# Optimization experiments

Hardware: AMD Instinct MI355X
Metric: run time of the kernel (lower is better)

The kernel has to match this reference:

```python
import jax, jax.numpy as jnp
import numpy as np

N_NODES = 50000
N_EDGES = 1600000
D = 128  # in_channels == hidden_channels


def _sage_conv(x, src, dst, W_l, W_r, b, n_nodes):
    # PyG SAGEConv (mean aggr): out = lin_l(mean_{j in N(i)} x_j) + lin_r(x_i)
    msg = x[src]                                              # [E, d] gather
    agg = jax.ops.segment_sum(msg, dst, num_segments=n_nodes)  # [N, d]
    deg = jax.ops.segment_sum(jnp.ones((src.shape[0],), x.dtype), dst,
                              num_segments=n_nodes)            # [N]
    mean = agg / jnp.maximum(deg, 1.0)[:, None]
    return mean @ W_l.T + b + x @ W_r.T


def setup_inputs() -> dict:
    key = jax.random.key(0)
    ks = jax.random.split(key, 8)
    x = jax.random.normal(ks[0], (N_NODES, D), dtype=jnp.float32)
    edge_index = jax.random.randint(ks[1], (2, N_EDGES), 0, N_NODES, dtype=jnp.int32)
    s = 1.0 / np.sqrt(D)
    W1_l = jax.random.uniform(ks[2], (D, D), jnp.float32, -s, s)
    W1_r = jax.random.uniform(ks[3], (D, D), jnp.float32, -s, s)
    b1 = jnp.zeros((D,), jnp.float32)
    W2_l = jax.random.uniform(ks[4], (D, D), jnp.float32, -s, s)
    W2_r = jax.random.uniform(ks[5], (D, D), jnp.float32, -s, s)
    b2 = jnp.zeros((D,), jnp.float32)
    return {"x": x, "edge_index": edge_index,
            "W1_l": W1_l, "W1_r": W1_r, "b1": b1,
            "W2_l": W2_l, "W2_r": W2_r, "b2": b2}


def reference(x, edge_index, W1_l, W1_r, b1, W2_l, W2_r, b2):
    src, dst = edge_index[0], edge_index[1]
    n = x.shape[0]
    # layer 1: conv -> relu (dropout is identity in eval mode)
    h = jax.nn.relu(_sage_conv(x, src, dst, W1_l, W1_r, b1, n))
    # layer 2
    h = jax.nn.relu(_sage_conv(h, src, dst, W2_l, W2_r, b2, n))
    return h
```

## Files before the change

### kernel.cpp

```cpp
#include <hip/hip_runtime.h>

#define D 128
#define BW_LOG 6
#define BWID 64
#define CAP 4096
#define CHUNK 4096
#define NB_MAX 1024

typedef unsigned short u16;
typedef unsigned int u32;
typedef __attribute__((ext_vector_type(8))) short bf16x8;
typedef __attribute__((ext_vector_type(8))) unsigned short u16x8;
typedef __attribute__((ext_vector_type(4))) float f32x4;

__device__ __forceinline__ float bf2f(u16 h) { return __uint_as_float(((u32)h) << 16); }
__device__ __forceinline__ u16 f2bf(float f) {
    u32 u = __float_as_uint(f);
    u32 r = (u + 0x7fffu + ((u >> 16) & 1u)) >> 16;
    return (u16)r;
}


__global__ __launch_bounds__(256)
void prep_kernel(const float* __restrict__ x, u16* __restrict__ xb, int n4,
                 const float* __restrict__ W1l, const float* __restrict__ W1r,
                 const float* __restrict__ W2l, const float* __restrict__ W2r,
                 u16* __restrict__ wc1, u16* __restrict__ wc2,
                 const int* __restrict__ dst, int* __restrict__ gh,
                 int E, int nb, int nblk, int xblk) {
    __shared__ int h[NB_MAX];
    int b = blockIdx.x;
    int t = threadIdx.x;
    if (b < xblk) {
        int i = b * 256 + t;
        if (i < n4) {
            float4 v = ((const float4*)x)[i];
            ushort4 o;
            o.x = f2bf(v.x); o.y = f2bf(v.y); o.z = f2bf(v.z); o.w = f2bf(v.w);
            ((ushort4*)xb)[i] = o;
        }
        return;
    }
    if (b < xblk + 256) {
        int wb = b - xblk;
        int n = wb & 127;
        const float* Wl = (wb < 128) ? W1l : W2l;
        const float* Wr = (wb < 128) ? W1r : W2r;
        u16* wcat = (wb < 128) ? wc1 : wc2;
        float v = (t < 128) ? Wl[n * 128 + t] : Wr[n * 128 + t - 128];
        wcat[n * 256 + t] = f2bf(v);
        return;
    }
    int hb = b - xblk - 256;
    for (int i = t; i < nb; i += 256) h[i] = 0;
    __syncthreads();
    int lo = hb * CHUNK, hi = min(lo + CHUNK, E);
    for (int i = lo + t; i < hi; i += 256) atomicAdd(&h[dst[i] >> BW_LOG], 1);
    __syncthreads();
    for (int i = t; i < nb; i += 256) gh[(size_t)i * nblk + hb] = h[i];
}


__global__ __launch_bounds__(64)
void part_scan1_kernel(int* __restrict__ gh, int* __restrict__ btot, int nblk) {
    int k = blockIdx.x;
    int t = threadIdx.x;
    int* row = gh + (size_t)k * nblk;
    int chunk = (nblk + 63) >> 6;
    int lo = t * chunk, hi = min(lo + chunk, nblk);
    int s = 0;
    for (int i = lo; i < hi; ++i) s += row[i];
    int incl = s;
#pragma unroll
    for (int d2 = 1; d2 < 64; d2 <<= 1) { int u = __shfl_up(incl, d2, 64); if (t >= d2) incl += u; }
    int excl = incl - s;
    for (int i = lo; i < hi; ++i) { int c = row[i]; row[i] = excl; excl += c; }
    if (t == 63) btot[k] = incl;
}

__global__ __launch_bounds__(1024)
void part_scan2_kernel(const int* __restrict__ btot, int* __restrict__ bbase,
                       int nb, int* __restrict__ offN) {
    __shared__ int ws[16];
    int t = threadIdx.x, lane = t & 63, wid = t >> 6;
    int v = (t < nb) ? btot[t] : 0;
    int incl = v;
#pragma unroll
    for (int d2 = 1; d2 < 64; d2 <<= 1) { int u = __shfl_up(incl, d2, 64); if (lane >= d2) incl += u; }
    if (lane == 63) ws[wid] = incl;
    __syncthreads();
    if (wid == 0) {
        int w = (lane < 16) ? ws[lane] : 0;
#pragma unroll
        for (int d2 = 1; d2 < 16; d2 <<= 1) { int u = __shfl_up(w, d2, 64); if (lane >= d2) w += u; }
        if (lane < 16) ws[lane] = w;
    }
    __syncthreads();
    int base = wid ? ws[wid - 1] : 0;
    int excl = base + incl - v;
    if (t < nb) bbase[t] = excl;
    if (t == nb - 1) { bbase[nb] = excl + v; *offN = excl + v; }
}

__global__ __launch_bounds__(256)
void part_scatter_kernel(const int* __restrict__ src, const int* __restrict__ dst,
                         const int* __restrict__ gh, const int* __restrict__ bbase,
                         u32* __restrict__ ebuf, int E, int nb, int nblk) {
    __shared__ int cur[NB_MAX];
    int b = blockIdx.x;
    for (int i = threadIdx.x; i < nb; i += 256)
        cur[i] = bbase[i] + gh[(size_t)i * nblk + b];
    __syncthreads();
    int lo = b * CHUNK, hi = min(lo + CHUNK, E);
    for (int i = lo + threadIdx.x; i < hi; i += 256) {
        int d = dst[i];
        int p = atomicAdd(&cur[d >> BW_LOG], 1);
        ebuf[p] = ((u32)(d & (BWID - 1)) << 16) | (u32)src[i];
    }
}

__global__ __launch_bounds__(256)
void bucket_sort_kernel(u32* __restrict__ ebuf, const int* __restrict__ bbase,
                        int* __restrict__ off, int n_nodes) {
    __shared__ u32 in_s[CAP];
    __shared__ u16 out_s[CAP];
    __shared__ int hist[BWID], cur[BWID];
    int b = blockIdx.x;
    int base = bbase[b];
    int n_b = bbase[b + 1] - base;
    int t = threadIdx.x;
    if (t < BWID) hist[t] = 0;
    for (int i = t; i < n_b && i < CAP; i += 256) in_s[i] = ebuf[base + i];
    __syncthreads();
    for (int i = t; i < n_b && i < CAP; i += 256) atomicAdd(&hist[in_s[i] >> 16], 1);
    __syncthreads();
    if (t < BWID) {
        int s = hist[t];
        int incl = s;
#pragma unroll
        for (int d2 = 1; d2 < 64; d2 <<= 1) { int u = __shfl_up(incl, d2, 64); if (t >= d2) incl += u; }
        int excl = incl - s;
        cur[t] = excl;
        int node = (b << BW_LOG) + t;
        if (node < n_nodes) off[node] = base + excl;
    }
    __syncthreads();
    for (int i = t; i < n_b && i < CAP; i += 256) {
        u32 v = in_s[i];
        int p = atomicAdd(&cur[v >> 16], 1);
        if (p < CAP) out_s[p] = (u16)(v & 0xffffu);
    }
    __syncthreads();
    for (int i = t; i < n_b && i < CAP; i += 256) ebuf[base + i] = (u32)out_s[i];
}


__global__ __launch_bounds__(256)
void aggregate_bf16_kernel(const u16* __restrict__ xb, const int* __restrict__ off,
                           const u32* __restrict__ eidx, u16* __restrict__ meanb,
                           int n_nodes) {
    int node = blockIdx.x * 8 + (threadIdx.x >> 5);
    int lane = threadIdx.x & 31;
    if (node >= n_nodes) return;
    int beg = off[node], end = off[node + 1];
    int c = lane * 4;

    float ax = 0.f, ay = 0.f, az = 0.f, aw = 0.f;
    int e = beg;
    for (; e + 8 <= end; e += 8) {
        ushort4 v0 = *(const ushort4*)&xb[(size_t)eidx[e + 0] * D + c];
        ushort4 v1 = *(const ushort4*)&xb[(size_t)eidx[e + 1] * D + c];
        ushort4 v2 = *(const ushort4*)&xb[(size_t)eidx[e + 2] * D + c];
        ushort4 v3 = *(const ushort4*)&xb[(size_t)eidx[e + 3] * D + c];
        ushort4 v4 = *(const ushort4*)&xb[(size_t)eidx[e + 4] * D + c];
        ushort4 v5 = *(const ushort4*)&xb[(size_t)eidx[e + 5] * D + c];
        ushort4 v6 = *(const ushort4*)&xb[(size_t)eidx[e + 6] * D + c];
        ushort4 v7 = *(const ushort4*)&xb[(size_t)eidx[e + 7] * D + c];
        ax += bf2f(v0.x) + bf2f(v1.x) + bf2f(v2.x) + bf2f(v3.x)
            + bf2f(v4.x) + bf2f(v5.x) + bf2f(v6.x) + bf2f(v7.x);
        ay += bf2f(v0.y) + bf2f(v1.y) + bf2f(v2.y) + bf2f(v3.y)
            + bf2f(v4.y) + bf2f(v5.y) + bf2f(v6.y) + bf2f(v7.y);
        az += bf2f(v0.z) + bf2f(v1.z) + bf2f(v2.z) + bf2f(v3.z)
            + bf2f(v4.z) + bf2f(v5.z) + bf2f(v6.z) + bf2f(v7.z);
        aw += bf2f(v0.w) + bf2f(v1.w) + bf2f(v2.w) + bf2f(v3.w)
            + bf2f(v4.w) + bf2f(v5.w) + bf2f(v6.w) + bf2f(v7.w);
    }
    for (; e < end; ++e) {
        ushort4 v = *(const ushort4*)&xb[(size_t)eidx[e] * D + c];
        ax += bf2f(v.x); ay += bf2f(v.y); az += bf2f(v.z); aw += bf2f(v.w);
    }

    int deg = end - beg;
    float inv = 1.f / (float)(deg > 0 ? deg : 1);
    ushort4 o;
    o.x = f2bf(ax * inv); o.y = f2bf(ay * inv); o.z = f2bf(az * inv); o.w = f2bf(aw * inv);
    *(ushort4*)&meanb[(size_t)node * D + c] = o;
}


template<bool OUT_BF16>
__global__ __launch_bounds__(512)
void linear_mfma_kernel(const u16* __restrict__ Amean, const u16* __restrict__ Aself,
                        const u16* __restrict__ Wc, const float* __restrict__ bias,
                        void* __restrict__ outp, int N) {
    __shared__ u16 ws[128][136];

    int t = threadIdx.x;
    int l = t & 63;
    int wv = t >> 6;
    int m0 = blockIdx.x * 128 + wv * 16;
    int lr = l & 15;
    int kg = (l >> 4) * 8;
    int rowA = m0 + lr;
    int rc = rowA < N ? rowA : N - 1;
    const u16* r1 = Amean + (size_t)rc * D;
    const u16* r2 = Aself + (size_t)rc * D;

    bf16x8 a[8];
#pragma unroll
    for (int kt = 0; kt < 4; ++kt) {
        a[kt]     = *(const bf16x8*)(r1 + kt * 32 + kg);
        a[kt + 4] = *(const bf16x8*)(r2 + kt * 32 + kg);
    }

    f32x4 acc[8];
#pragma unroll
    for (int nt = 0; nt < 8; ++nt) acc[nt] = (f32x4){0.f, 0.f, 0.f, 0.f};

    for (int half = 0; half < 2; ++half) {
        if (half) __syncthreads();
        for (int i = t; i < 2048; i += 512) {
            int n = i >> 4, kq = i & 15;
            *(u16x8*)&ws[n][kq * 8] = *(const u16x8*)&Wc[(size_t)n * 256 + half * 128 + kq * 8];
        }
        __syncthreads();

#pragma unroll
        for (int nt = 0; nt < 8; ++nt) {
            bf16x8 b0 = *(const bf16x8*)&ws[nt * 16 + lr][0 * 32 + kg];
            bf16x8 b1 = *(const bf16x8*)&ws[nt * 16 + lr][1 * 32 + kg];
            bf16x8 b2 = *(const bf16x8*)&ws[nt * 16 + lr][2 * 32 + kg];
            bf16x8 b3 = *(const bf16x8*)&ws[nt * 16 + lr][3 * 32 + kg];
            acc[nt] = __builtin_amdgcn_mfma_f32_16x16x32_bf16(a[half * 4 + 0], b0, acc[nt], 0, 0, 0);
            acc[nt] = __builtin_amdgcn_mfma_f32_16x16x32_bf16(a[half * 4 + 1], b1, acc[nt], 0, 0, 0);
            acc[nt] = __builtin_amdgcn_mfma_f32_16x16x32_bf16(a[half * 4 + 2], b2, acc[nt], 0, 0, 0);
            acc[nt] = __builtin_amdgcn_mfma_f32_16x16x32_bf16(a[half * 4 + 3], b3, acc[nt], 0, 0, 0);
        }
    }

#pragma unroll
    for (int nt = 0; nt < 8; ++nt) {
        int col = nt * 16 + lr;
        float bb = bias[col];
#pragma unroll
        for (int j = 0; j < 4; ++j) {
            int r = m0 + (l >> 4) * 4 + j;
            if (r < N) {
                float v = fmaxf(acc[nt][j] + bb, 0.f);
                if (OUT_BF16) ((u16*)outp)[(size_t)r * D + col] = f2bf(v);
                else          ((float*)outp)[(size_t)r * D + col] = v;
            }
        }
    }
}

extern "C" void kernel_launch(void* const* d_in, const int* in_sizes, int n_in,
                              void* d_out, int out_size, void* d_ws, size_t ws_size,
                              hipStream_t stream) {
    const float* x   = (const float*)d_in[0];
    const int*   ei  = (const int*)d_in[1];
    const float* W1l = (const float*)d_in[2];
    const float* W1r = (const float*)d_in[3];
    const float* b1  = (const float*)d_in[4];
    const float* W2l = (const float*)d_in[5];
    const float* W2r = (const float*)d_in[6];
    const float* b2  = (const float*)d_in[7];
    float* out = (float*)d_out;

    const int N = in_sizes[0] / D;
    const int E = in_sizes[1] / 2;
    const int* src = ei;
    const int* dst = ei + E;
    const int NB = (N + BWID - 1) >> BW_LOG;
    const int NBLK = (E + CHUNK - 1) / CHUNK;
    const int N4 = N * D / 4;
    const int XBLK = (N4 + 255) / 256;

    char* wp_ = (char*)d_ws;
    auto alloc = [&](size_t bytes) { char* p = wp_; wp_ += (bytes + 63) & ~(size_t)63; return p; };
    int* off_p   = (int*)alloc((size_t)(N + 1) * 4);
    int* bbase_p = (int*)alloc((size_t)(NB + 1) * 4);
    int* btot_p  = (int*)alloc((size_t)NB * 4);
    int* gh_p    = (int*)alloc((size_t)NB * NBLK * 4);
    u32* ebuf_p  = (u32*)alloc((size_t)E * 4);
    u16* xb      = (u16*)alloc((size_t)N * D * 2);
    u16* meanb   = (u16*)alloc((size_t)N * D * 2);
    u16* h1b     = (u16*)alloc((size_t)N * D * 2);
    u16* wc1     = (u16*)alloc((size_t)128 * 256 * 2);
    u16* wc2     = (u16*)alloc((size_t)128 * 256 * 2);

    prep_kernel<<<XBLK + 256 + NBLK, 256, 0, stream>>>(
        x, xb, N4, W1l, W1r, W2l, W2r, wc1, wc2, dst, gh_p, E, NB, NBLK, XBLK);

    part_scan1_kernel<<<NB, 64, 0, stream>>>(gh_p, btot_p, NBLK);
    part_scan2_kernel<<<1, 1024, 0, stream>>>(btot_p, bbase_p, NB, off_p + N);
    part_scatter_kernel<<<NBLK, 256, 0, stream>>>(src, dst, gh_p, bbase_p, ebuf_p, E, NB, NBLK);
    bucket_sort_kernel<<<NB, 256, 0, stream>>>(ebuf_p, bbase_p, off_p, N);

    aggregate_bf16_kernel<<<(N + 7) / 8, 256, 0, stream>>>(xb, off_p, ebuf_p, meanb, N);
    linear_mfma_kernel<true><<<(N + 127) / 128, 512, 0, stream>>>(meanb, xb, wc1, b1, h1b, N);

    aggregate_bf16_kernel<<<(N + 7) / 8, 256, 0, stream>>>(h1b, off_p, ebuf_p, meanb, N);
    linear_mfma_kernel<false><<<(N + 127) / 128, 512, 0, stream>>>(meanb, h1b, wc2, b2, out, N);
}
```

Baseline: 213.4 us.

## Split feature matrices into two 64-column halves and aggregate each half separately

Stores node features, means and hidden activations as two separate 64-column bf16 planes and runs the neighbour aggregation twice, once per plane, with 16 lanes per node. Each gathered plane is about 6.4 MB, so the aim is for the working set of each random gather pass to fit better in L2/MALL and raise cache hit rates. In exchange the edge index list is read twice per layer, there are extra kernel launches, and each gathered row segment is only 128 bytes.

```diff
diff --git a/kernel.cpp b/kernel.cpp
--- a/kernel.cpp
+++ b/kernel.cpp
@@ -1,6 +1,7 @@
 #include <hip/hip_runtime.h>
 
 #define D 128
+#define DH 64
 #define BW_LOG 6
 #define BWID 64
 #define CAP 4096
@@ -22,7 +23,8 @@
 
 
 __global__ __launch_bounds__(256)
-void prep_kernel(const float* __restrict__ x, u16* __restrict__ xb, int n4,
+void prep_kernel(const float* __restrict__ x, u16* __restrict__ xb0, u16* __restrict__ xb1,
+                 int n4,
                  const float* __restrict__ W1l, const float* __restrict__ W1r,
                  const float* __restrict__ W2l, const float* __restrict__ W2r,
                  u16* __restrict__ wc1, u16* __restrict__ wc2,
@@ -37,7 +39,11 @@
             float4 v = ((const float4*)x)[i];
             ushort4 o;
             o.x = f2bf(v.x); o.y = f2bf(v.y); o.z = f2bf(v.z); o.w = f2bf(v.w);
-            ((ushort4*)xb)[i] = o;
+            int n = i >> 5;
+            int d0 = (i & 31) * 4;
+            u16* dstp = (d0 < DH) ? (xb0 + (size_t)n * DH + d0)
+                                  : (xb1 + (size_t)n * DH + d0 - DH);
+            *(ushort4*)dstp = o;
         }
         return;
     }
@@ -156,11 +162,11 @@
 
 
 __global__ __launch_bounds__(256)
-void aggregate_bf16_kernel(const u16* __restrict__ xb, const int* __restrict__ off,
-                           const u32* __restrict__ eidx, u16* __restrict__ meanb,
+void aggregate_half_kernel(const u16* __restrict__ xh, const int* __restrict__ off,
+                           const u32* __restrict__ eidx, u16* __restrict__ mh,
                            int n_nodes) {
-    int node = blockIdx.x * 8 + (threadIdx.x >> 5);
-    int lane = threadIdx.x & 31;
+    int node = blockIdx.x * 16 + (threadIdx.x >> 4);
+    int lane = threadIdx.x & 15;
     if (node >= n_nodes) return;
     int beg = off[node], end = off[node + 1];
     int c = lane * 4;
@@ -168,14 +174,14 @@
     float ax = 0.f, ay = 0.f, az = 0.f, aw = 0.f;
     int e = beg;
     for (; e + 8 <= end; e += 8) {
-        ushort4 v0 = *(const ushort4*)&xb[(size_t)eidx[e + 0] * D + c];
-        ushort4 v1 = *(const ushort4*)&xb[(size_t)eidx[e + 1] * D + c];
-        ushort4 v2 = *(const ushort4*)&xb[(size_t)eidx[e + 2] * D + c];
-        ushort4 v3 = *(const ushort4*)&xb[(size_t)eidx[e + 3] * D + c];
-        ushort4 v4 = *(const ushort4*)&xb[(size_t)eidx[e + 4] * D + c];
-        ushort4 v5 = *(const ushort4*)&xb[(size_t)eidx[e + 5] * D + c];
-        ushort4 v6 = *(const ushort4*)&xb[(size_t)eidx[e + 6] * D + c];
-        ushort4 v7 = *(const ushort4*)&xb[(size_t)eidx[e + 7] * D + c];
+        ushort4 v0 = *(const ushort4*)&xh[(size_t)eidx[e + 0] * DH + c];
+        ushort4 v1 = *(const ushort4*)&xh[(size_t)eidx[e + 1] * DH + c];
+        ushort4 v2 = *(const ushort4*)&xh[(size_t)eidx[e + 2] * DH + c];
+        ushort4 v3 = *(const ushort4*)&xh[(size_t)eidx[e + 3] * DH + c];
+        ushort4 v4 = *(const ushort4*)&xh[(size_t)eidx[e + 4] * DH + c];
+        ushort4 v5 = *(const ushort4*)&xh[(size_t)eidx[e + 5] * DH + c];
+        ushort4 v6 = *(const ushort4*)&xh[(size_t)eidx[e + 6] * DH + c];
+        ushort4 v7 = *(const ushort4*)&xh[(size_t)eidx[e + 7] * DH + c];
         ax += bf2f(v0.x) + bf2f(v1.x) + bf2f(v2.x) + bf2f(v3.x)
             + bf2f(v4.x) + bf2f(v5.x) + bf2f(v6.x) + bf2f(v7.x);
         ay += bf2f(v0.y) + bf2f(v1.y) + bf2f(v2.y) + bf2f(v3.y)
@@ -186,7 +192,7 @@
             + bf2f(v4.w) + bf2f(v5.w) + bf2f(v6.w) + bf2f(v7.w);
     }
     for (; e < end; ++e) {
-        ushort4 v = *(const ushort4*)&xb[(size_t)eidx[e] * D + c];
+        ushort4 v = *(const ushort4*)&xh[(size_t)eidx[e] * DH + c];
         ax += bf2f(v.x); ay += bf2f(v.y); az += bf2f(v.z); aw += bf2f(v.w);
     }
 
@@ -194,15 +200,16 @@
     float inv = 1.f / (float)(deg > 0 ? deg : 1);
     ushort4 o;
     o.x = f2bf(ax * inv); o.y = f2bf(ay * inv); o.z = f2bf(az * inv); o.w = f2bf(aw * inv);
-    *(ushort4*)&meanb[(size_t)node * D + c] = o;
+    *(ushort4*)&mh[(size_t)node * DH + c] = o;
 }
 
 
 template<bool OUT_BF16>
 __global__ __launch_bounds__(512)
-void linear_mfma_kernel(const u16* __restrict__ Amean, const u16* __restrict__ Aself,
+void linear_mfma_kernel(const u16* __restrict__ Am0, const u16* __restrict__ Am1,
+                        const u16* __restrict__ As0, const u16* __restrict__ As1,
                         const u16* __restrict__ Wc, const float* __restrict__ bias,
-                        void* __restrict__ outp, int N) {
+                        void* __restrict__ o0, void* __restrict__ o1, int N) {
     __shared__ u16 ws[128][136];
 
     int t = threadIdx.x;
@@ -213,15 +220,16 @@
     int kg = (l >> 4) * 8;
     int rowA = m0 + lr;
     int rc = rowA < N ? rowA : N - 1;
-    const u16* r1 = Amean + (size_t)rc * D;
-    const u16* r2 = Aself + (size_t)rc * D;
 
     bf16x8 a[8];
-#pragma unroll
-    for (int kt = 0; kt < 4; ++kt) {
-        a[kt]     = *(const bf16x8*)(r1 + kt * 32 + kg);
-        a[kt + 4] = *(const bf16x8*)(r2 + kt * 32 + kg);
-    }
+    a[0] = *(const bf16x8*)(Am0 + (size_t)rc * DH + kg);
+    a[1] = *(const bf16x8*)(Am0 + (size_t)rc * DH + 32 + kg);
+    a[2] = *(const bf16x8*)(Am1 + (size_t)rc * DH + kg);
+    a[3] = *(const bf16x8*)(Am1 + (size_t)rc * DH + 32 + kg);
+    a[4] = *(const bf16x8*)(As0 + (size_t)rc * DH + kg);
+    a[5] = *(const bf16x8*)(As0 + (size_t)rc * DH + 32 + kg);
+    a[6] = *(const bf16x8*)(As1 + (size_t)rc * DH + kg);
+    a[7] = *(const bf16x8*)(As1 + (size_t)rc * DH + 32 + kg);
 
     f32x4 acc[8];
 #pragma unroll
@@ -257,8 +265,12 @@
             int r = m0 + (l >> 4) * 4 + j;
             if (r < N) {
                 float v = fmaxf(acc[nt][j] + bb, 0.f);
-                if (OUT_BF16) ((u16*)outp)[(size_t)r * D + col] = f2bf(v);
-                else          ((float*)outp)[(size_t)r * D + col] = v;
+                if (OUT_BF16) {
+                    if (col < DH) ((u16*)o0)[(size_t)r * DH + col] = f2bf(v);
+                    else          ((u16*)o1)[(size_t)r * DH + col - DH] = f2bf(v);
+                } else {
+                    ((float*)o0)[(size_t)r * D + col] = v;
+                }
             }
         }
     }
@@ -293,23 +305,32 @@
     int* btot_p  = (int*)alloc((size_t)NB * 4);
     int* gh_p    = (int*)alloc((size_t)NB * NBLK * 4);
     u32* ebuf_p  = (u32*)alloc((size_t)E * 4);
-    u16* xb      = (u16*)alloc((size_t)N * D * 2);
-    u16* meanb   = (u16*)alloc((size_t)N * D * 2);
-    u16* h1b     = (u16*)alloc((size_t)N * D * 2);
+    u16* xb0     = (u16*)alloc((size_t)N * DH * 2);
+    u16* xb1     = (u16*)alloc((size_t)N * DH * 2);
+    u16* mean0   = (u16*)alloc((size_t)N * DH * 2);
+    u16* mean1   = (u16*)alloc((size_t)N * DH * 2);
+    u16* h1b0    = (u16*)alloc((size_t)N * DH * 2);
+    u16* h1b1    = (u16*)alloc((size_t)N * DH * 2);
     u16* wc1     = (u16*)alloc((size_t)128 * 256 * 2);
     u16* wc2     = (u16*)alloc((size_t)128 * 256 * 2);
 
     prep_kernel<<<XBLK + 256 + NBLK, 256, 0, stream>>>(
-        x, xb, N4, W1l, W1r, W2l, W2r, wc1, wc2, dst, gh_p, E, NB, NBLK, XBLK);
+        x, xb0, xb1, N4, W1l, W1r, W2l, W2r, wc1, wc2, dst, gh_p, E, NB, NBLK, XBLK);
 
     part_scan1_kernel<<<NB, 64, 0, stream>>>(gh_p, btot_p, NBLK);
     part_scan2_kernel<<<1, 1024, 0, stream>>>(btot_p, bbase_p, NB, off_p + N);
     part_scatter_kernel<<<NBLK, 256, 0, stream>>>(src, dst, gh_p, bbase_p, ebuf_p, E, NB, NBLK);
     bucket_sort_kernel<<<NB, 256, 0, stream>>>(ebuf_p, bbase_p, off_p, N);
 
-    aggregate_bf16_kernel<<<(N + 7) / 8, 256, 0, stream>>>(xb, off_p, ebuf_p, meanb, N);
-    linear_mfma_kernel<true><<<(N + 127) / 128, 512, 0, stream>>>(meanb, xb, wc1, b1, h1b, N);
-
-    aggregate_bf16_kernel<<<(N + 7) / 8, 256, 0, stream>>>(h1b, off_p, ebuf_p, meanb, N);
-    linear_mfma_kernel<false><<<(N + 127) / 128, 512, 0, stream>>>(meanb, h1b, wc2, b2, out, N);
-}
+    const int AGRID = (N + 15) / 16;
+
+    aggregate_half_kernel<<<AGRID, 256, 0, stream>>>(xb0, off_p, ebuf_p, mean0, N);
+    aggregate_half_kernel<<<AGRID, 256, 0, stream>>>(xb1, off_p, ebuf_p, mean1, N);
+    linear_mfma_kernel<true><<<(N + 127) / 128, 512, 0, stream>>>(
+        mean0, mean1, xb0, xb1, wc1, b1, h1b0, h1b1, N);
+
+    aggregate_half_kernel<<<AGRID, 256, 0, stream>>>(h1b0, off_p, ebuf_p, mean0, N);
+    aggregate_half_kernel<<<AGRID, 256, 0, stream>>>(h1b1, off_p, ebuf_p, mean1, N);
+    linear_mfma_kernel<false><<<(N + 127) / 128, 512, 0, stream>>>(
+        mean0, mean1, h1b0, h1b1, wc2, b2, out, nullptr, N);
+}
```

Result: slower. 224.2 us (+5.0%).
